# Kernel optimization log

Hardware: AMD Instinct MI355X
Metric: run time of the kernel (lower is better)

The kernel has to match this reference:

```python
import jax, jax.numpy as jnp
import numpy as np

B, N, M, L, H = 32, 4096, 256, 128, 4
GAMMA = 2.0


def setup_inputs() -> dict:
    key = jax.random.key(0)
    kx, km, kv, ku, kw = jax.random.split(key, 5)
    x = jax.random.normal(kx, (B, N, M), dtype=jnp.float32)
    masks = (jax.random.uniform(km, (B, N)) > 0.3).astype(jnp.float32)
    # VarianceScaling(scale=0.1, fan_in, uniform) ~ small init; exact dist doesn't affect math
    V = jax.random.normal(kv, (H, M, L), dtype=jnp.float32) * 0.02
    U = jax.random.normal(ku, (H, M, L), dtype=jnp.float32) * 0.02
    w = jax.random.normal(kw, (H, L, 1), dtype=jnp.float32) * 0.05
    return {"x": x, "masks": masks, "V": V, "U": U, "w": w}


def reference(x, masks, V, U, w):
    # x: [B,N,M], masks: [B,N], V/U: [H,M,L], w: [H,L,1]
    m = masks[:, None, :, None]  # [B,1,N,1] broadcast over heads
    gated = jnp.tanh(jnp.einsum('bnm,hml->bhnl', x, V)) * jax.nn.sigmoid(
        jnp.einsum('bnm,hml->bhnl', x, U))          # [B,H,N,L]
    logits = jnp.einsum('bhnl,hl->bhn', gated, w[..., 0])[..., None]  # [B,H,N,1]
    a = m * logits                                   # masked logits (as in original)
    a = m * jnp.exp(a)                               # masked exp
    a = a / jnp.sum(a, axis=2, keepdims=True)        # softmax over instances
    ag = a ** GAMMA
    a = ag / jnp.sum(ag, axis=2, keepdims=True)      # gamma-power renorm
    emb = jnp.einsum('bhnk,bnm->bhm', a, x)          # weighted sum; k is the trailing 1
    emb = emb.reshape(B, H * M)                      # concat heads along axis=1
    att = jnp.transpose(a, (1, 0, 2, 3))             # [H,B,N,1] (per-head attention list)
    return (att, emb)
```

## Files before the change

### kernel.cpp

```cpp
#include <hip/hip_runtime.h>
#include <hip/hip_bf16.h>
#include <stdint.h>

#define B_ 32
#define N_ 4096
#define M_ 256
#define L_ 128
#define H_ 4
#define BN_ (B_ * N_)

typedef __bf16 bf16x8 __attribute__((ext_vector_type(8)));
typedef float  f32x4  __attribute__((ext_vector_type(4)));

__device__ __forceinline__ unsigned short f2bf(float f) {
    unsigned int u = __float_as_uint(f);
    u += 0x7fffu + ((u >> 16) & 1u);
    return (unsigned short)(u >> 16);
}
__device__ __forceinline__ unsigned int pack2(float lo, float hi) {
    return (unsigned int)f2bf(lo) | ((unsigned int)f2bf(hi) << 16);
}

__device__ __forceinline__ void gload16(const void* g, void* l) {
    __builtin_amdgcn_global_load_lds(
        (const __attribute__((address_space(1))) unsigned int*)g,
        (__attribute__((address_space(3))) unsigned int*)l, 16, 0, 0);
}

__global__ void prep_vu_img(const float* __restrict__ V, const float* __restrict__ U,
                            unsigned short* __restrict__ vu) {
    __shared__ float slab[64][129];
    const int b   = blockIdx.x;
    const int mat = b & 1, ks = (b >> 1) & 3, h = b >> 3;
    const float* src = (mat ? U : V) + ((size_t)h * M_ + ks * 64) * L_;
    const float scale = mat ? -1.0f : 2.0f;
    const int tid = threadIdx.x;
#pragma unroll
    for (int rep = 0; rep < 32; ++rep) {
        int idx = rep * 256 + tid;
        slab[idx >> 7][idx & 127] = scale * src[(size_t)(idx >> 7) * L_ + (idx & 127)];
    }
    __syncthreads();
#pragma unroll
    for (int rep = 0; rep < 4; ++rep) {
        int cidx = rep * 256 + tid;
        int l  = cidx >> 3;
        int kk = (cidx & 7) * 8;
        uint4 o;
        o.x = pack2(slab[kk + 0][l], slab[kk + 1][l]);
        o.y = pack2(slab[kk + 2][l], slab[kk + 3][l]);
        o.z = pack2(slab[kk + 4][l], slab[kk + 5][l]);
        o.w = pack2(slab[kk + 6][l], slab[kk + 7][l]);
        int tl = kk >> 5, kl = kk & 31;
        char* dst = (char*)vu + (((size_t)(h * 8 + ks * 2 + tl)) * 2 + mat) * 8192;
        int byte = (l * 64 + kl * 2) ^ ((l & 14) << 3);
        *(uint4*)(dst + byte) = o;
    }
}

__global__ __launch_bounds__(256, 2)
void gemm_fast8(const float* __restrict__ x,
                const unsigned short* __restrict__ vu,
                const float* __restrict__ w,
                float* __restrict__ logits) {
    __shared__ __align__(16) float          xs[2][4096];
    __shared__ __align__(16) unsigned short vs[2][4096];
    __shared__ __align__(16) unsigned short us[2][4096];
    __shared__ float part[2][128];

    const int orig    = blockIdx.x;
    const int logical = (orig & 7) * 512 + (orig >> 3);
    const int tile    = logical >> 2;
    const int h       = logical & 3;

    const int tid  = threadIdx.x;
    const int lane = tid & 63;
    const int wv   = tid >> 6;
    const int g    = lane >> 4;
    const int c    = lane & 15;
    const int wr   = wv & 1;
    const int wc   = wv >> 1;

    f32x4 accV[4][4], accU[4][4];
#pragma unroll
    for (int rf = 0; rf < 4; ++rf)
#pragma unroll
        for (int cf = 0; cf < 4; ++cf) {
            accV[rf][cf] = (f32x4){0.f, 0.f, 0.f, 0.f};
            accU[rf][cf] = (f32x4){0.f, 0.f, 0.f, 0.f};
        }

    const int soff = wv * 2048;

    const char* gvs = (const char*)vu + (size_t)h * 131072 + soff + lane * 16;
    const char* gus = gvs + 8192;

    const int cb = ((lane & 7) * 16) ^ ((lane >> 3) << 4);
    const char* gxl = (const char*)x
        + ((size_t)tile * 128 + wv * 32 + (lane >> 3)) * 1024 + cb;

    int aoff[4], boff[4];
#pragma unroll
    for (int rf = 0; rf < 4; ++rf) {
        int r = wr * 64 + rf * 16 + c;
        aoff[rf] = (r * 128 + g * 32) ^ ((r & 7) << 4);
    }
#pragma unroll
    for (int cf = 0; cf < 4; ++cf) {
        int l = wc * 64 + cf * 16 + c;
        boff[cf] = (l * 64 + g * 16) ^ ((l & 14) << 3);
    }

#define SCHED __builtin_amdgcn_sched_barrier(0)

#define STAGEX(t, bufi) do {                                         \
        const char* _g = gxl + (t) * 128;                            \
        char* _d = (char*)xs[bufi] + wv * 4096;                      \
        gload16(_g,          _d);                                    \
        gload16(_g + 8192,   _d + 1024);                             \
        gload16(_g + 16384,  _d + 2048);                             \
        gload16(_g + 24576,  _d + 3072);                             \
    } while (0)

#define STAGEB(t, bufi) do {                                         \
        const char* _gv = gvs + (t) * 16384;                         \
        const char* _gu = gus + (t) * 16384;                         \
        gload16(_gv,        (char*)vs[bufi] + soff);                 \
        gload16(_gv + 1024, (char*)vs[bufi] + soff + 1024);          \
        gload16(_gu,        (char*)us[bufi] + soff);                 \
        gload16(_gu + 1024, (char*)us[bufi] + soff + 1024);          \
    } while (0)

    STAGEX(0, 0);
    STAGEB(0, 0);
    SCHED;

#pragma unroll
    for (int t = 0; t < 8; ++t) {
        asm volatile("s_waitcnt vmcnt(0)" ::: "memory");
        __builtin_amdgcn_s_barrier();
        SCHED;

        if (t < 7) {
            STAGEX(t + 1, (t + 1) & 1);
            STAGEB(t + 1, (t + 1) & 1);
        }
        SCHED;

        const int buf = t & 1;
        const float* xbuf = xs[buf];
        const char*  vbuf = (const char*)vs[buf];
        const char*  ubuf = (const char*)us[buf];

        bf16x8 bv[4], bu[4];
#pragma unroll
        for (int cf = 0; cf < 4; ++cf) {
            bv[cf] = *(const bf16x8*)(vbuf + boff[cf]);
            bu[cf] = *(const bf16x8*)(ubuf + boff[cf]);
        }
        __builtin_amdgcn_s_setprio(1);
#pragma unroll
        for (int rf = 0; rf < 4; ++rf) {
            f32x4 p = *(const f32x4*)((const char*)xbuf + aoff[rf]);
            f32x4 q = *(const f32x4*)((const char*)xbuf + (aoff[rf] ^ 16));
            bf16x8 a;
            a[0] = (__bf16)p.x; a[1] = (__bf16)p.y;
            a[2] = (__bf16)p.z; a[3] = (__bf16)p.w;
            a[4] = (__bf16)q.x; a[5] = (__bf16)q.y;
            a[6] = (__bf16)q.z; a[7] = (__bf16)q.w;
#pragma unroll
            for (int cf = 0; cf < 4; ++cf) {
                accV[rf][cf] = __builtin_amdgcn_mfma_f32_16x16x32_bf16(a, bv[cf], accV[rf][cf], 0, 0, 0);
                accU[rf][cf] = __builtin_amdgcn_mfma_f32_16x16x32_bf16(a, bu[cf], accU[rf][cf], 0, 0, 0);
            }
        }
        __builtin_amdgcn_s_setprio(0);
    }
#undef STAGEB
#undef STAGEX
#undef SCHED

    const float* wrow = w + h * L_ + wc * 64;
#pragma unroll
    for (int rf = 0; rf < 4; ++rf) {
        float plog[4] = {0.f, 0.f, 0.f, 0.f};
#pragma unroll
        for (int cf = 0; cf < 4; ++cf) {
            float wvv = wrow[cf * 16 + c];
#pragma unroll
            for (int i = 0; i < 4; ++i) {
                float A = __expf(accV[rf][cf][i]);
                float E = __expf(accU[rf][cf][i]);
                float gg = __fdividef(A - 1.f, (A + 1.f) * (1.f + E));
                plog[i] += gg * wvv;
            }
        }
#pragma unroll
        for (int i = 0; i < 4; ++i) {
            float v = plog[i];
            v += __shfl_xor(v, 1);
            v += __shfl_xor(v, 2);
            v += __shfl_xor(v, 4);
            v += __shfl_xor(v, 8);
            if (c == 0)
                part[wc][wr * 64 + rf * 16 + g * 4 + i] = v;
        }
    }
    __syncthreads();
    if (tid < 128) {
        float v = part[0][tid] + part[1][tid];
        int rowflat = tile * 128 + tid;
        int b = rowflat >> 12;
        int n = rowflat & (N_ - 1);
        logits[((size_t)b * H_ + h) * N_ + n] = v;
    }
}

__global__ void prep_vu_slow(const float* __restrict__ V, const float* __restrict__ U,
                             unsigned short* __restrict__ Vt, unsigned short* __restrict__ Ut) {
    int idx = blockIdx.x * 256 + threadIdx.x;
    int m = idx & (M_ - 1);
    int l = (idx >> 8) & (L_ - 1);
    int h = idx >> 15;
    Vt[idx] = f2bf(V[((size_t)h * M_ + m) * L_ + l]);
    Ut[idx] = f2bf(U[((size_t)h * M_ + m) * L_ + l]);
}

#define BM 128
#define BK 64

__global__ __launch_bounds__(256, 2)
void gemm_logits(const float* __restrict__ x,
                 const unsigned short* __restrict__ Vt,
                 const unsigned short* __restrict__ Ut,
                 const float* __restrict__ w,
                 float* __restrict__ logits) {
    __shared__ __align__(16) unsigned short xs[BM * BK];
    __shared__ __align__(16) unsigned short vs[L_ * BK];
    __shared__ __align__(16) unsigned short us[L_ * BK];
    __shared__ float wl[L_];

    const int h    = blockIdx.x >> 10;
    const int tile = blockIdx.x & 1023;
    const int row0 = tile * BM;
    const int tid  = threadIdx.x;
    const int lane = tid & 63;
    const int wave = tid >> 6;

    if (tid < L_) wl[tid] = w[h * L_ + tid];

    f32x4 accV[2][8], accU[2][8];
#pragma unroll
    for (int rf = 0; rf < 2; ++rf)
#pragma unroll
        for (int cf = 0; cf < 8; ++cf) {
            accV[rf][cf] = (f32x4){0.f, 0.f, 0.f, 0.f};
            accU[rf][cf] = (f32x4){0.f, 0.f, 0.f, 0.f};
        }

    const unsigned short* Vh = Vt + (size_t)h * L_ * M_;
    const unsigned short* Uh = Ut + (size_t)h * L_ * M_;
    const int g = lane >> 4;
    const int c = lane & 15;

    for (int ks = 0; ks < 4; ++ks) {
        const int k0 = ks * BK;
        __syncthreads();
#pragma unroll
        for (int p = 0; p < 4; ++p) {
            int row = p * 32 + (tid >> 3);
            int kk  = (tid & 7) * 8;
            const float* gx = x + (size_t)(row0 + row) * M_ + k0 + kk;
            float4 a = *(const float4*)gx;
            float4 b = *(const float4*)(gx + 4);
            uint4 o;
            o.x = pack2(a.x, a.y); o.y = pack2(a.z, a.w);
            o.z = pack2(b.x, b.y); o.w = pack2(b.z, b.w);
            int byte = (row * BK + kk) * 2;
            byte ^= (row & 7) << 4;
            *(uint4*)((char*)xs + byte) = o;
        }
#pragma unroll
        for (int p = 0; p < 4; ++p) {
            int l  = p * 32 + (tid >> 3);
            int kk = (tid & 7) * 8;
            uint4 v = *(const uint4*)(Vh + (size_t)l * M_ + k0 + kk);
            uint4 u = *(const uint4*)(Uh + (size_t)l * M_ + k0 + kk);
            int byte = (l * BK + kk) * 2;
            byte ^= (l & 7) << 4;
            *(uint4*)((char*)vs + byte) = v;
            *(uint4*)((char*)us + byte) = u;
        }
        __syncthreads();
#pragma unroll
        for (int ksub = 0; ksub < 2; ++ksub) {
            bf16x8 afr[2];
#pragma unroll
            for (int rf = 0; rf < 2; ++rf) {
                int row = wave * 32 + rf * 16 + c;
                int byte = (row * BK + ksub * 32 + g * 8) * 2;
                byte ^= (row & 7) << 4;
                afr[rf] = *(const bf16x8*)((const char*)xs + byte);
            }
#pragma unroll
            for (int cf = 0; cf < 8; ++cf) {
                int l = cf * 16 + c;
                int byte = (l * BK + ksub * 32 + g * 8) * 2;
                byte ^= (l & 7) << 4;
                bf16x8 bv = *(const bf16x8*)((const char*)vs + byte);
                bf16x8 bu = *(const bf16x8*)((const char*)us + byte);
#pragma unroll
                for (int rf = 0; rf < 2; ++rf) {
                    accV[rf][cf] = __builtin_amdgcn_mfma_f32_16x16x32_bf16(afr[rf], bv, accV[rf][cf], 0, 0, 0);
                    accU[rf][cf] = __builtin_amdgcn_mfma_f32_16x16x32_bf16(afr[rf], bu, accU[rf][cf], 0, 0, 0);
                }
            }
        }
    }
#pragma unroll
    for (int rf = 0; rf < 2; ++rf) {
        float plog[4] = {0.f, 0.f, 0.f, 0.f};
#pragma unroll
        for (int cf = 0; cf < 8; ++cf) {
            float wvv = wl[cf * 16 + c];
#pragma unroll
            for (int i = 0; i < 4; ++i) {
                float vv = accV[rf][cf][i];
                float uu = accU[rf][cf][i];
                vv = fminf(fmaxf(vv, -20.f), 20.f);
                float e2v = __expf(2.f * vv);
                float t = __fdividef(e2v - 1.f, e2v + 1.f);
                float s = __fdividef(1.f, 1.f + __expf(-uu));
                plog[i] += t * s * wvv;
            }
        }
#pragma unroll
        for (int i = 0; i < 4; ++i) {
            float v = plog[i];
            v += __shfl_xor(v, 1);
            v += __shfl_xor(v, 2);
            v += __shfl_xor(v, 4);
            v += __shfl_xor(v, 8);
            if (c == 0) {
                int rowflat = row0 + wave * 32 + rf * 16 + g * 4 + i;
                int b = rowflat >> 12;
                int n = rowflat & (N_ - 1);
                logits[((size_t)b * H_ + h) * N_ + n] = v;
            }
        }
    }
}

__global__ __launch_bounds__(256)
void softmax_att(const float* __restrict__ logits, const float* __restrict__ masks,
                 float* __restrict__ att) {
    const int bh = blockIdx.x;
    const int b = bh >> 2, h = bh & 3;
    __shared__ float e2s[N_];
    __shared__ float red[4];
    const int tid = threadIdx.x;

    float sum = 0.f;
#pragma unroll
    for (int i = 0; i < N_ / 256; ++i) {
        int n = i * 256 + tid;
        float lg = logits[((size_t)b * H_ + h) * N_ + n];
        float mv = masks[(size_t)b * N_ + n];
        float e = mv * __expf(mv * lg);
        float e2 = e * e;
        e2s[n] = e2;
        sum += e2;
    }
#pragma unroll
    for (int off = 32; off >= 1; off >>= 1) sum += __shfl_xor(sum, off);
    if ((tid & 63) == 0) red[tid >> 6] = sum;
    __syncthreads();
    float S = red[0] + red[1] + red[2] + red[3];
    float inv = 1.f / S;
#pragma unroll
    for (int i = 0; i < N_ / 256; ++i) {
        int n = i * 256 + tid;
        att[((size_t)h * B_ + b) * N_ + n] = e2s[n] * inv;
    }
}

#define NCH 32
#define CHUNK (N_ / NCH)

__global__ __launch_bounds__(256)
void emb_partial(const float* __restrict__ x, const float* __restrict__ att,
                 float* __restrict__ part) {
    const int bc = blockIdx.x;
    const int b = bc >> 5, ch = bc & 31;
    __shared__ float as[H_][CHUNK];
    const int tid = threadIdx.x;

    for (int i = tid; i < H_ * CHUNK; i += 256) {
        int hh = i >> 7;
        int j  = i & (CHUNK - 1);
        as[hh][j] = att[((size_t)hh * B_ + b) * N_ + ch * CHUNK + j];
    }
    __syncthreads();

    float a0 = 0.f, a1 = 0.f, a2 = 0.f, a3 = 0.f;
    const float* xp = x + ((size_t)b * N_ + ch * CHUNK) * M_ + tid;
#pragma unroll 4
    for (int j = 0; j < CHUNK; ++j) {
        float xv = xp[(size_t)j * M_];
        a0 += as[0][j] * xv;
        a1 += as[1][j] * xv;
        a2 += as[2][j] * xv;
        a3 += as[3][j] * xv;
    }
    float* pp = part + (size_t)bc * H_ * M_ + tid;
    pp[0 * M_] = a0; pp[1 * M_] = a1; pp[2 * M_] = a2; pp[3 * M_] = a3;
}

__global__ __launch_bounds__(256)
void emb_reduce(const float* __restrict__ part, float* __restrict__ emb) {
    int idx = blockIdx.x * 256 + threadIdx.x;
    int b = idx >> 10;
    int r = idx & 1023;
    float s = 0.f;
#pragma unroll
    for (int ci = 0; ci < NCH; ++ci)
        s += part[((size_t)(b * NCH + ci)) * (H_ * M_) + r];
    emb[idx] = s;
}

extern "C" void kernel_launch(void* const* d_in, const int* in_sizes, int n_in,
                              void* d_out, int out_size, void* d_ws, size_t ws_size,
                              hipStream_t stream) {
    const float* x     = (const float*)d_in[0];
    const float* masks = (const float*)d_in[1];
    const float* V     = (const float*)d_in[2];
    const float* U     = (const float*)d_in[3];
    const float* w     = (const float*)d_in[4];

    float* att = (float*)d_out;
    float* emb = att + (size_t)H_ * B_ * N_;

    char* ws = (char*)d_ws;
    const size_t VU_BYTES  = (size_t)64 * 8192;
    const size_t LG_BYTES  = (size_t)B_ * H_ * N_ * 4;
    const size_t PT_BYTES  = (size_t)B_ * NCH * H_ * M_ * 4;
    const size_t NEED_FAST = VU_BYTES + LG_BYTES + PT_BYTES;

    float* logits;
    float* partp;

    if (ws_size >= NEED_FAST) {
        unsigned short* vuimg = (unsigned short*)ws;
        logits = (float*)(ws + VU_BYTES);
        partp  = (float*)(ws + VU_BYTES + LG_BYTES);

        prep_vu_img<<<32,   256, 0, stream>>>(V, U, vuimg);
        gemm_fast8 <<<4096, 256, 0, stream>>>(x, vuimg, w, logits);
    } else {
        unsigned short* Vt = (unsigned short*)ws;
        unsigned short* Ut = (unsigned short*)(ws + 262144);
        logits = (float*)(ws + 524288);
        partp  = (float*)(ws + 524288 + LG_BYTES);

        prep_vu_slow<<<512, 256, 0, stream>>>(V, U, Vt, Ut);
        gemm_logits <<<4096, 256, 0, stream>>>(x, Vt, Ut, w, logits);
    }

    softmax_att<<<B_ * H_,              256, 0, stream>>>(logits, masks, att);
    emb_partial<<<B_ * NCH,             256, 0, stream>>>(x, att, partp);
    emb_reduce <<<(B_ * H_ * M_) / 256, 256, 0, stream>>>(partp, emb);
}
```

Measured before the change: 168.7 us.

## Split GEMM over L halves per block, write partial logits, sum in softmax

New measurement: 159.9 us. 5.2% less time.

```diff
diff --git a/kernel.cpp b/kernel.cpp
--- a/kernel.cpp
+++ b/kernel.cpp
@@ -27,8 +27,8 @@
         (__attribute__((address_space(3))) unsigned int*)l, 16, 0, 0);
 }
 
-__global__ void prep_vu_img(const float* __restrict__ V, const float* __restrict__ U,
-                            unsigned short* __restrict__ vu) {
+__global__ void prep_vu_img2(const float* __restrict__ V, const float* __restrict__ U,
+                             unsigned short* __restrict__ vu) {
     __shared__ float slab[64][129];
     const int b   = blockIdx.x;
     const int mat = b & 1, ks = (b >> 1) & 3, h = b >> 3;
@@ -52,83 +52,79 @@
         o.z = pack2(slab[kk + 4][l], slab[kk + 5][l]);
         o.w = pack2(slab[kk + 6][l], slab[kk + 7][l]);
         int tl = kk >> 5, kl = kk & 31;
-        char* dst = (char*)vu + (((size_t)(h * 8 + ks * 2 + tl)) * 2 + mat) * 8192;
-        int byte = (l * 64 + kl * 2) ^ ((l & 14) << 3);
+        int lh = l >> 6, ll = l & 63;
+        char* dst = (char*)vu
+            + ((((size_t)(h * 2 + lh) * 8 + (ks * 2 + tl)) * 2) + mat) * 4096;
+        int byte = (ll * 64 + kl * 2) ^ ((ll & 14) << 3);
         *(uint4*)(dst + byte) = o;
     }
 }
 
-__global__ __launch_bounds__(256, 2)
-void gemm_fast8(const float* __restrict__ x,
-                const unsigned short* __restrict__ vu,
-                const float* __restrict__ w,
-                float* __restrict__ logits) {
+__global__ __launch_bounds__(256, 3)
+void gemm_fast10(const float* __restrict__ x,
+                 const unsigned short* __restrict__ vu,
+                 const float* __restrict__ w,
+                 float* __restrict__ partL) {
     __shared__ __align__(16) float          xs[2][4096];
-    __shared__ __align__(16) unsigned short vs[2][4096];
-    __shared__ __align__(16) unsigned short us[2][4096];
-    __shared__ float part[2][128];
+    __shared__ __align__(16) unsigned short vs[2][2048];
+    __shared__ __align__(16) unsigned short us[2][2048];
 
     const int orig    = blockIdx.x;
-    const int logical = (orig & 7) * 512 + (orig >> 3);
-    const int tile    = logical >> 2;
-    const int h       = logical & 3;
+    const int logical = (orig & 7) * 1024 + (orig >> 3);
+    const int tile    = logical >> 3;
+    const int h       = (logical >> 1) & 3;
+    const int lh      = logical & 1;
 
     const int tid  = threadIdx.x;
     const int lane = tid & 63;
     const int wv   = tid >> 6;
     const int g    = lane >> 4;
     const int c    = lane & 15;
-    const int wr   = wv & 1;
-    const int wc   = wv >> 1;
-
-    f32x4 accV[4][4], accU[4][4];
-#pragma unroll
-    for (int rf = 0; rf < 4; ++rf)
+
+    f32x4 accV[2][4], accU[2][4];
+#pragma unroll
+    for (int rf = 0; rf < 2; ++rf)
 #pragma unroll
         for (int cf = 0; cf < 4; ++cf) {
             accV[rf][cf] = (f32x4){0.f, 0.f, 0.f, 0.f};
             accU[rf][cf] = (f32x4){0.f, 0.f, 0.f, 0.f};
         }
 
-    const int soff = wv * 2048;
-
-    const char* gvs = (const char*)vu + (size_t)h * 131072 + soff + lane * 16;
-    const char* gus = gvs + 8192;
-
-    const int cb = ((lane & 7) * 16) ^ ((lane >> 3) << 4);
-    const char* gxl = (const char*)x
-        + ((size_t)tile * 128 + wv * 32 + (lane >> 3)) * 1024 + cb;
-
-    int aoff[4], boff[4];
-#pragma unroll
-    for (int rf = 0; rf < 4; ++rf) {
-        int r = wr * 64 + rf * 16 + c;
-        aoff[rf] = (r * 128 + g * 32) ^ ((r & 7) << 4);
+    const char* gvs = (const char*)vu + (size_t)(h * 2 + lh) * 65536
+                      + wv * 1024 + lane * 16;
+    const char* gus = gvs + 4096;
+
+    const int offb = ((lane & 7) << 4) ^ (((lane >> 3) & 6) << 3);
+    const char* pA = (const char*)x
+        + ((size_t)tile * 128 + wv * 32 + (lane >> 3)) * 1024 + offb;
+    const char* pB = (const char*)x
+        + ((size_t)tile * 128 + wv * 32 + (lane >> 3)) * 1024 + (offb ^ 64);
+
+    int aoff[2], boff[4];
+#pragma unroll
+    for (int rf = 0; rf < 2; ++rf) {
+        int r = wv * 32 + rf * 16 + c;
+        aoff[rf] = (r * 128 + g * 32) ^ ((c & 14) << 3);
     }
 #pragma unroll
     for (int cf = 0; cf < 4; ++cf) {
-        int l = wc * 64 + cf * 16 + c;
-        boff[cf] = (l * 64 + g * 16) ^ ((l & 14) << 3);
+        int ll = cf * 16 + c;
+        boff[cf] = (ll * 64 + g * 16) ^ ((ll & 14) << 3);
     }
 
 #define SCHED __builtin_amdgcn_sched_barrier(0)
 
-#define STAGEX(t, bufi) do {                                         \
-        const char* _g = gxl + (t) * 128;                            \
-        char* _d = (char*)xs[bufi] + wv * 4096;                      \
-        gload16(_g,          _d);                                    \
-        gload16(_g + 8192,   _d + 1024);                             \
-        gload16(_g + 16384,  _d + 2048);                             \
-        gload16(_g + 24576,  _d + 3072);                             \
+#define STAGEX(t, bufi) do {                                             \
+        char* _d = (char*)xs[bufi] + wv * 4096;                          \
+        gload16(pA +     (t) * 128, _d);                                 \
+        gload16(pB + 8192  + (t) * 128, _d + 1024);                      \
+        gload16(pA + 16384 + (t) * 128, _d + 2048);                      \
+        gload16(pB + 24576 + (t) * 128, _d + 3072);                      \
     } while (0)
 
-#define STAGEB(t, bufi) do {                                         \
-        const char* _gv = gvs + (t) * 16384;                         \
-        const char* _gu = gus + (t) * 16384;                         \
-        gload16(_gv,        (char*)vs[bufi] + soff);                 \
-        gload16(_gv + 1024, (char*)vs[bufi] + soff + 1024);          \
-        gload16(_gu,        (char*)us[bufi] + soff);                 \
-        gload16(_gu + 1024, (char*)us[bufi] + soff + 1024);          \
+#define STAGEB(t, bufi) do {                                             \
+        gload16(gvs + (t) * 8192, (char*)vs[bufi] + wv * 1024);          \
+        gload16(gus + (t) * 8192, (char*)us[bufi] + wv * 1024);          \
     } while (0)
 
     STAGEX(0, 0);
@@ -148,31 +144,34 @@
         SCHED;
 
         const int buf = t & 1;
-        const float* xbuf = xs[buf];
-        const char*  vbuf = (const char*)vs[buf];
-        const char*  ubuf = (const char*)us[buf];
-
-        bf16x8 bv[4], bu[4];
+        const char* xbuf = (const char*)xs[buf];
+        const char* vbuf = (const char*)vs[buf];
+        const char* ubuf = (const char*)us[buf];
+
+        bf16x8 a0, a1;
+        {
+            f32x4 p = *(const f32x4*)(xbuf + aoff[0]);
+            f32x4 q = *(const f32x4*)(xbuf + (aoff[0] ^ 16));
+            a0[0] = (__bf16)p.x; a0[1] = (__bf16)p.y;
+            a0[2] = (__bf16)p.z; a0[3] = (__bf16)p.w;
+            a0[4] = (__bf16)q.x; a0[5] = (__bf16)q.y;
+            a0[6] = (__bf16)q.z; a0[7] = (__bf16)q.w;
+            p = *(const f32x4*)(xbuf + aoff[1]);
+            q = *(const f32x4*)(xbuf + (aoff[1] ^ 16));
+            a1[0] = (__bf16)p.x; a1[1] = (__bf16)p.y;
+            a1[2] = (__bf16)p.z; a1[3] = (__bf16)p.w;
+            a1[4] = (__bf16)q.x; a1[5] = (__bf16)q.y;
+            a1[6] = (__bf16)q.z; a1[7] = (__bf16)q.w;
+        }
+        __builtin_amdgcn_s_setprio(1);
 #pragma unroll
         for (int cf = 0; cf < 4; ++cf) {
-            bv[cf] = *(const bf16x8*)(vbuf + boff[cf]);
-            bu[cf] = *(const bf16x8*)(ubuf + boff[cf]);
-        }
-        __builtin_amdgcn_s_setprio(1);
-#pragma unroll
-        for (int rf = 0; rf < 4; ++rf) {
-            f32x4 p = *(const f32x4*)((const char*)xbuf + aoff[rf]);
-            f32x4 q = *(const f32x4*)((const char*)xbuf + (aoff[rf] ^ 16));
-            bf16x8 a;
-            a[0] = (__bf16)p.x; a[1] = (__bf16)p.y;
-            a[2] = (__bf16)p.z; a[3] = (__bf16)p.w;
-            a[4] = (__bf16)q.x; a[5] = (__bf16)q.y;
-            a[6] = (__bf16)q.z; a[7] = (__bf16)q.w;
-#pragma unroll
-            for (int cf = 0; cf < 4; ++cf) {
-                accV[rf][cf] = __builtin_amdgcn_mfma_f32_16x16x32_bf16(a, bv[cf], accV[rf][cf], 0, 0, 0);
-                accU[rf][cf] = __builtin_amdgcn_mfma_f32_16x16x32_bf16(a, bu[cf], accU[rf][cf], 0, 0, 0);
-            }
+            bf16x8 bv = *(const bf16x8*)(vbuf + boff[cf]);
+            bf16x8 bu = *(const bf16x8*)(ubuf + boff[cf]);
+            accV[0][cf] = __builtin_amdgcn_mfma_f32_16x16x32_bf16(a0, bv, accV[0][cf], 0, 0, 0);
+            accV[1][cf] = __builtin_amdgcn_mfma_f32_16x16x32_bf16(a1, bv, accV[1][cf], 0, 0, 0);
+            accU[0][cf] = __builtin_amdgcn_mfma_f32_16x16x32_bf16(a0, bu, accU[0][cf], 0, 0, 0);
+            accU[1][cf] = __builtin_amdgcn_mfma_f32_16x16x32_bf16(a1, bu, accU[1][cf], 0, 0, 0);
         }
         __builtin_amdgcn_s_setprio(0);
     }
@@ -180,9 +179,10 @@
 #undef STAGEX
 #undef SCHED
 
-    const float* wrow = w + h * L_ + wc * 64;
-#pragma unroll
-    for (int rf = 0; rf < 4; ++rf) {
+    const float* wrow = w + h * L_ + lh * 64;
+    float* pl = partL + (size_t)lh * (B_ * H_ * N_);
+#pragma unroll
+    for (int rf = 0; rf < 2; ++rf) {
         float plog[4] = {0.f, 0.f, 0.f, 0.f};
 #pragma unroll
         for (int cf = 0; cf < 4; ++cf) {
@@ -202,17 +202,13 @@
             v += __shfl_xor(v, 2);
             v += __shfl_xor(v, 4);
             v += __shfl_xor(v, 8);
-            if (c == 0)
-                part[wc][wr * 64 + rf * 16 + g * 4 + i] = v;
-        }
-    }
-    __syncthreads();
-    if (tid < 128) {
-        float v = part[0][tid] + part[1][tid];
-        int rowflat = tile * 128 + tid;
-        int b = rowflat >> 12;
-        int n = rowflat & (N_ - 1);
-        logits[((size_t)b * H_ + h) * N_ + n] = v;
+            if (c == 0) {
+                int rowflat = tile * 128 + wv * 32 + rf * 16 + g * 4 + i;
+                int b = rowflat >> 12;
+                int n = rowflat & (N_ - 1);
+                pl[((size_t)b * H_ + h) * N_ + n] = v;
+            }
+        }
     }
 }
 
@@ -352,6 +348,40 @@
 }
 
 __global__ __launch_bounds__(256)
+void softmax_att2(const float* __restrict__ pl0, const float* __restrict__ pl1,
+                  const float* __restrict__ masks, float* __restrict__ att) {
+    const int bh = blockIdx.x;
+    const int b = bh >> 2, h = bh & 3;
+    __shared__ float e2s[N_];
+    __shared__ float red[4];
+    const int tid = threadIdx.x;
+
+    float sum = 0.f;
+#pragma unroll
+    for (int i = 0; i < N_ / 256; ++i) {
+        int n = i * 256 + tid;
+        size_t idx = ((size_t)b * H_ + h) * N_ + n;
+        float lg = pl0[idx] + pl1[idx];
+        float mv = masks[(size_t)b * N_ + n];
+        float e = mv * __expf(mv * lg);
+        float e2 = e * e;
+        e2s[n] = e2;
+        sum += e2;
+    }
+#pragma unroll
+    for (int off = 32; off >= 1; off >>= 1) sum += __shfl_xor(sum, off);
+    if ((tid & 63) == 0) red[tid >> 6] = sum;
+    __syncthreads();
+    float S = red[0] + red[1] + red[2] + red[3];
+    float inv = 1.f / S;
+#pragma unroll
+    for (int i = 0; i < N_ / 256; ++i) {
+        int n = i * 256 + tid;
+        att[((size_t)h * B_ + b) * N_ + n] = e2s[n] * inv;
+    }
+}
+
+__global__ __launch_bounds__(256)
 void softmax_att(const float* __restrict__ logits, const float* __restrict__ masks,
                  float* __restrict__ att) {
     const int bh = blockIdx.x;
@@ -441,32 +471,33 @@
     float* emb = att + (size_t)H_ * B_ * N_;
 
     char* ws = (char*)d_ws;
-    const size_t VU_BYTES  = (size_t)64 * 8192;
-    const size_t LG_BYTES  = (size_t)B_ * H_ * N_ * 4;
+    const size_t VU_BYTES  = (size_t)128 * 4096;
+    const size_t PL_BYTES  = (size_t)2 * B_ * H_ * N_ * 4;
     const size_t PT_BYTES  = (size_t)B_ * NCH * H_ * M_ * 4;
-    const size_t NEED_FAST = VU_BYTES + LG_BYTES + PT_BYTES;
-
-    float* logits;
-    float* partp;
+    const size_t NEED_FAST = VU_BYTES + PL_BYTES + PT_BYTES;
 
     if (ws_size >= NEED_FAST) {
         unsigned short* vuimg = (unsigned short*)ws;
-        logits = (float*)(ws + VU_BYTES);
-        partp  = (float*)(ws + VU_BYTES + LG_BYTES);
-
-        prep_vu_img<<<32,   256, 0, stream>>>(V, U, vuimg);
-        gemm_fast8 <<<4096, 256, 0, stream>>>(x, vuimg, w, logits);
+        float* partL = (float*)(ws + VU_BYTES);
+        float* partp = (float*)(ws + VU_BYTES + PL_BYTES);
+
+        prep_vu_img2<<<32,   256, 0, stream>>>(V, U, vuimg);
+        gemm_fast10 <<<8192, 256, 0, stream>>>(x, vuimg, w, partL);
+        softmax_att2<<<B_ * H_, 256, 0, stream>>>(partL,
+                                                  partL + (size_t)B_ * H_ * N_,
+                                                  masks, att);
+        emb_partial<<<B_ * NCH, 256, 0, stream>>>(x, att, partp);
+        emb_reduce <<<(B_ * H_ * M_) / 256, 256, 0, stream>>>(partp, emb);
     } else {
         unsigned short* Vt = (unsigned short*)ws;
         unsigned short* Ut = (unsigned short*)(ws + 262144);
-        logits = (float*)(ws + 524288);
-        partp  = (float*)(ws + 524288 + LG_BYTES);
+        float* logits = (float*)(ws + 524288);
+        float* partp  = (float*)(ws + 524288 + (size_t)B_ * H_ * N_ * 4);
 
         prep_vu_slow<<<512, 256, 0, stream>>>(V, U, Vt, Ut);
         gemm_logits <<<4096, 256, 0, stream>>>(x, Vt, Ut, w, logits);
-    }
-
-    softmax_att<<<B_ * H_,              256, 0, stream>>>(logits, masks, att);
-    emb_partial<<<B_ * NCH,             256, 0, stream>>>(x, att, partp);
-    emb_reduce <<<(B_ * H_ * M_) / 256, 256, 0, stream>>>(partp, emb);
-}
+        softmax_att <<<B_ * H_, 256, 0, stream>>>(logits, masks, att);
+        emb_partial <<<B_ * NCH, 256, 0, stream>>>(x, att, partp);
+        emb_reduce  <<<(B_ * H_ * M_) / 256, 256, 0, stream>>>(partp, emb);
+    }
+}
```

## Use 512-thread blocks with single-buffered x tile to raise occupancy

Applied to the files above, without the earlier changes.

New measurement: 458.5 us. 2.72x slower.

```diff
diff --git a/kernel.cpp b/kernel.cpp
--- a/kernel.cpp
+++ b/kernel.cpp
@@ -58,12 +58,12 @@
     }
 }
 
-__global__ __launch_bounds__(256, 2)
-void gemm_fast8(const float* __restrict__ x,
-                const unsigned short* __restrict__ vu,
-                const float* __restrict__ w,
-                float* __restrict__ logits) {
-    __shared__ __align__(16) float          xs[2][4096];
+__global__ __launch_bounds__(512, 6)
+void gemm_fast12(const float* __restrict__ x,
+                 const unsigned short* __restrict__ vu,
+                 const float* __restrict__ w,
+                 float* __restrict__ logits) {
+    __shared__ __align__(16) float          xs[4096];
     __shared__ __align__(16) unsigned short vs[2][4096];
     __shared__ __align__(16) unsigned short us[2][4096];
     __shared__ float part[2][128];
@@ -78,60 +78,53 @@
     const int wv   = tid >> 6;
     const int g    = lane >> 4;
     const int c    = lane & 15;
-    const int wr   = wv & 1;
-    const int wc   = wv >> 1;
-
-    f32x4 accV[4][4], accU[4][4];
-#pragma unroll
-    for (int rf = 0; rf < 4; ++rf)
+    const int wr   = wv >> 1;
+    const int lhh  = wv & 1;
+
+    f32x4 accV[2][4], accU[2][4];
+#pragma unroll
+    for (int rf = 0; rf < 2; ++rf)
 #pragma unroll
         for (int cf = 0; cf < 4; ++cf) {
             accV[rf][cf] = (f32x4){0.f, 0.f, 0.f, 0.f};
             accU[rf][cf] = (f32x4){0.f, 0.f, 0.f, 0.f};
         }
 
-    const int soff = wv * 2048;
-
-    const char* gvs = (const char*)vu + (size_t)h * 131072 + soff + lane * 16;
+    const char* gvs = (const char*)vu + (size_t)h * 131072 + wv * 1024 + lane * 16;
     const char* gus = gvs + 8192;
 
-    const int cb = ((lane & 7) * 16) ^ ((lane >> 3) << 4);
-    const char* gxl = (const char*)x
-        + ((size_t)tile * 128 + wv * 32 + (lane >> 3)) * 1024 + cb;
-
-    int aoff[4], boff[4];
-#pragma unroll
-    for (int rf = 0; rf < 4; ++rf) {
-        int r = wr * 64 + rf * 16 + c;
-        aoff[rf] = (r * 128 + g * 32) ^ ((r & 7) << 4);
+    const int offb = ((lane & 7) << 4) ^ (((lane >> 3) & 6) << 3);
+    const char* pA = (const char*)x
+        + ((size_t)tile * 128 + wv * 16 + (lane >> 3)) * 1024 + offb;
+    const char* pB = (const char*)x
+        + ((size_t)tile * 128 + wv * 16 + 8 + (lane >> 3)) * 1024 + (offb ^ 64);
+
+    int aoff[2], boff[4];
+#pragma unroll
+    for (int rf = 0; rf < 2; ++rf) {
+        int r = wr * 32 + rf * 16 + c;
+        aoff[rf] = (r * 128 + g * 32) ^ ((r & 14) << 3);
     }
 #pragma unroll
     for (int cf = 0; cf < 4; ++cf) {
-        int l = wc * 64 + cf * 16 + c;
+        int l = lhh * 64 + cf * 16 + c;
         boff[cf] = (l * 64 + g * 16) ^ ((l & 14) << 3);
     }
 
 #define SCHED __builtin_amdgcn_sched_barrier(0)
 
-#define STAGEX(t, bufi) do {                                         \
-        const char* _g = gxl + (t) * 128;                            \
-        char* _d = (char*)xs[bufi] + wv * 4096;                      \
-        gload16(_g,          _d);                                    \
-        gload16(_g + 8192,   _d + 1024);                             \
-        gload16(_g + 16384,  _d + 2048);                             \
-        gload16(_g + 24576,  _d + 3072);                             \
+#define STAGEX(t) do {                                                   \
+        char* _d = (char*)xs + wv * 2048;                                \
+        gload16(pA + (t) * 128, _d);                                     \
+        gload16(pB + (t) * 128, _d + 1024);                              \
     } while (0)
 
-#define STAGEB(t, bufi) do {                                         \
-        const char* _gv = gvs + (t) * 16384;                         \
-        const char* _gu = gus + (t) * 16384;                         \
-        gload16(_gv,        (char*)vs[bufi] + soff);                 \
-        gload16(_gv + 1024, (char*)vs[bufi] + soff + 1024);          \
-        gload16(_gu,        (char*)us[bufi] + soff);                 \
-        gload16(_gu + 1024, (char*)us[bufi] + soff + 1024);          \
+#define STAGEB(t, bufi) do {                                             \
+        gload16(gvs + (t) * 16384, (char*)vs[bufi] + wv * 1024);         \
+        gload16(gus + (t) * 16384, (char*)us[bufi] + wv * 1024);         \
     } while (0)
 
-    STAGEX(0, 0);
+    STAGEX(0);
     STAGEB(0, 0);
     SCHED;
 
@@ -141,38 +134,45 @@
         __builtin_amdgcn_s_barrier();
         SCHED;
 
+        bf16x8 a0, a1;
+        {
+            f32x4 p = *(const f32x4*)((const char*)xs + aoff[0]);
+            f32x4 q = *(const f32x4*)((const char*)xs + (aoff[0] ^ 16));
+            a0[0] = (__bf16)p.x; a0[1] = (__bf16)p.y;
+            a0[2] = (__bf16)p.z; a0[3] = (__bf16)p.w;
+            a0[4] = (__bf16)q.x; a0[5] = (__bf16)q.y;
+            a0[6] = (__bf16)q.z; a0[7] = (__bf16)q.w;
+            p = *(const f32x4*)((const char*)xs + aoff[1]);
+            q = *(const f32x4*)((const char*)xs + (aoff[1] ^ 16));
+            a1[0] = (__bf16)p.x; a1[1] = (__bf16)p.y;
+            a1[2] = (__bf16)p.z; a1[3] = (__bf16)p.w;
+            a1[4] = (__bf16)q.x; a1[5] = (__bf16)q.y;
+            a1[6] = (__bf16)q.z; a1[7] = (__bf16)q.w;
+        }
+
         if (t < 7) {
-            STAGEX(t + 1, (t + 1) & 1);
+            asm volatile("s_waitcnt lgkmcnt(0)" ::: "memory");
+            SCHED;
+            __builtin_amdgcn_s_barrier();
+            SCHED;
+            STAGEX(t + 1);
             STAGEB(t + 1, (t + 1) & 1);
-        }
-        SCHED;
+            SCHED;
+        }
 
         const int buf = t & 1;
-        const float* xbuf = xs[buf];
-        const char*  vbuf = (const char*)vs[buf];
-        const char*  ubuf = (const char*)us[buf];
-
-        bf16x8 bv[4], bu[4];
+        const char* vbuf = (const char*)vs[buf];
+        const char* ubuf = (const char*)us[buf];
+
+        __builtin_amdgcn_s_setprio(1);
 #pragma unroll
         for (int cf = 0; cf < 4; ++cf) {
-            bv[cf] = *(const bf16x8*)(vbuf + boff[cf]);
-            bu[cf] = *(const bf16x8*)(ubuf + boff[cf]);
-        }
-        __builtin_amdgcn_s_setprio(1);
-#pragma unroll
-        for (int rf = 0; rf < 4; ++rf) {
-            f32x4 p = *(const f32x4*)((const char*)xbuf + aoff[rf]);
-            f32x4 q = *(const f32x4*)((const char*)xbuf + (aoff[rf] ^ 16));
-            bf16x8 a;
-            a[0] = (__bf16)p.x; a[1] = (__bf16)p.y;
-            a[2] = (__bf16)p.z; a[3] = (__bf16)p.w;
-            a[4] = (__bf16)q.x; a[5] = (__bf16)q.y;
-            a[6] = (__bf16)q.z; a[7] = (__bf16)q.w;
-#pragma unroll
-            for (int cf = 0; cf < 4; ++cf) {
-                accV[rf][cf] = __builtin_amdgcn_mfma_f32_16x16x32_bf16(a, bv[cf], accV[rf][cf], 0, 0, 0);
-                accU[rf][cf] = __builtin_amdgcn_mfma_f32_16x16x32_bf16(a, bu[cf], accU[rf][cf], 0, 0, 0);
-            }
+            bf16x8 bv = *(const bf16x8*)(vbuf + boff[cf]);
+            bf16x8 bu = *(const bf16x8*)(ubuf + boff[cf]);
+            accV[0][cf] = __builtin_amdgcn_mfma_f32_16x16x32_bf16(a0, bv, accV[0][cf], 0, 0, 0);
+            accV[1][cf] = __builtin_amdgcn_mfma_f32_16x16x32_bf16(a1, bv, accV[1][cf], 0, 0, 0);
+            accU[0][cf] = __builtin_amdgcn_mfma_f32_16x16x32_bf16(a0, bu, accU[0][cf], 0, 0, 0);
+            accU[1][cf] = __builtin_amdgcn_mfma_f32_16x16x32_bf16(a1, bu, accU[1][cf], 0, 0, 0);
         }
         __builtin_amdgcn_s_setprio(0);
     }
@@ -180,9 +180,9 @@
 #undef STAGEX
 #undef SCHED
 
-    const float* wrow = w + h * L_ + wc * 64;
-#pragma unroll
-    for (int rf = 0; rf < 4; ++rf) {
+    const float* wrow = w + h * L_ + lhh * 64;
+#pragma unroll
+    for (int rf = 0; rf < 2; ++rf) {
         float plog[4] = {0.f, 0.f, 0.f, 0.f};
 #pragma unroll
         for (int cf = 0; cf < 4; ++cf) {
@@ -203,7 +203,7 @@
             v += __shfl_xor(v, 4);
             v += __shfl_xor(v, 8);
             if (c == 0)
-                part[wc][wr * 64 + rf * 16 + g * 4 + i] = v;
+                part[lhh][wr * 32 + rf * 16 + g * 4 + i] = v;
         }
     }
     __syncthreads();
@@ -455,7 +455,7 @@
         partp  = (float*)(ws + VU_BYTES + LG_BYTES);
 
         prep_vu_img<<<32,   256, 0, stream>>>(V, U, vuimg);
-        gemm_fast8 <<<4096, 256, 0, stream>>>(x, vuimg, w, logits);
+        gemm_fast12<<<4096, 512, 0, stream>>>(x, vuimg, w, logits);
     } else {
         unsigned short* Vt = (unsigned short*)ws;
         unsigned short* Ut = (unsigned short*)(ws + 262144);
```
